# Kernel optimization log

Measured on AMD Instinct MI355X. Metric: run time of the kernel, lower is better.

The kernel has to match this reference:

```python
import jax, jax.numpy as jnp
import numpy as np

B, C, H, W = 64, 64, 128, 128
K = 7
PAD = 3


def setup_inputs() -> dict:
    key = jax.random.key(0)
    kx, kw, kb = jax.random.split(key, 3)
    scale = (C * K) ** (-0.5)
    x = jax.random.normal(kx, (B, C, H, W), dtype=jnp.float32)
    w = jax.random.normal(kw, (C, K, K), dtype=jnp.float32) * scale
    bias = jax.random.normal(kb, (1,), dtype=jnp.float32) * scale
    return {"x": x, "w": w, "bias": bias}


def reference(x, w, bias):
    # Single-output-channel 2D cross-correlation (sums over all input channels),
    # with zero padding PAD on both spatial dims, stride 1.
    # Matches the torch module's per-pixel loop: out[b, oh, ow] =
    #   sum_{c,dh,dw} x_pad[b, c, oh+dh, ow+dw] * w[c, dh, dw] + bias
    out = jax.lax.conv_general_dilated(
        x,                      # (B, C, H, W)
        w[None, :, :, :],       # (O=1, C, K, K)
        window_strides=(1, 1),
        padding=[(PAD, PAD), (PAD, PAD)],
        dimension_numbers=("NCHW", "OIHW", "NCHW"),
    )
    return out[:, 0] + bias  # (B, H_out, W_out)
```

## Files before the change

kernel.cpp:

```cpp
#include <hip/hip_runtime.h>
#include <stdint.h>


typedef short bf16x8 __attribute__((ext_vector_type(8)));
typedef float f32x4 __attribute__((ext_vector_type(4)));

#define HB    16
#define XS    20
#define XCOLS 134
#define XB1   (XCOLS * XS)
#define AROW  132
#define NSLOT 8

__device__ __forceinline__ uint32_t pk2bf(float a, float b) {
    uint32_t ua = __builtin_bit_cast(uint32_t, a);
    uint32_t ub = __builtin_bit_cast(uint32_t, b);
    ua += 0x7FFFu + ((ua >> 16) & 1u);
    ub += 0x7FFFu + ((ub >> 16) & 1u);
    return (ua >> 16) | (ub & 0xFFFF0000u);
}

__device__ __forceinline__ void lds_barrier() {
    asm volatile("s_waitcnt lgkmcnt(0)\n\ts_barrier" ::: "memory");
}

__global__ __launch_bounds__(256, 3)
void conv_v6(const float* __restrict__ x, const float* __restrict__ w,
             const float* __restrict__ bias, float* __restrict__ out) {
    __shared__ uint32_t xlds[2][2 * XB1];
    __shared__ float    acc[NSLOT * AROW];

    const int tid  = threadIdx.x;
    const int lane = tid & 63;
    const int wv   = tid >> 6;
    const int bx   = blockIdx.x;
    const int cs   = bx & 1;
    const int band = (bx >> 1) & 7;
    const int b    = bx >> 4;
    const int h0   = band * HB;
    const int r0   = h0 - 3;

    const int nl = lane & 15;
    const int q  = lane >> 4;

    for (int i = tid; i < NSLOT * AROW; i += 256) acc[i] = 0.f;
    for (int i = tid; i < 2 * 2 * 6 * XS; i += 256) {
        int bi   = i / (2 * 6 * XS);
        int rem  = i - bi * (2 * 6 * XS);
        int rs   = rem / (6 * XS);
        int rem2 = rem - rs * (6 * XS);
        int colh = rem2 / XS;
        int dwi  = rem2 - colh * XS;
        int col  = (colh < 3) ? colh : (128 + colh);
        xlds[bi][rs * XB1 + col * XS + dwi] = 0u;
    }

    bf16x8 Bf[7];
#pragma unroll
    for (int kk = 0; kk < 7; kk++) {
        bf16x8 f;
#pragma unroll
        for (int j = 0; j < 8; j++) {
            float v = (nl < 7) ? w[(32 * cs + 8 * q + j) * 49 + nl * 7 + kk] : 0.f;
            uint32_t u = __builtin_bit_cast(uint32_t, v);
            u += 0x7FFFu + ((u >> 16) & 1u);
            f[j] = (short)(u >> 16);
        }
        Bf[kk] = f;
    }

    const int cgrp = tid & 3;
    const int rsel = tid >> 7;
    const int colq = (tid >> 2) & 31;
    const float4* xp4 =
        (const float4*)x + ((size_t)b * 64 + 32 * cs + 8 * cgrp) * 4096;

    float4 pre[8];

    {
        const int r = r0 + rsel;
        const bool v = ((unsigned)r < 128u);
        const int base = r * 32 + colq;
#pragma unroll
        for (int i = 0; i < 8; i++) {
            float4 g = {0.f, 0.f, 0.f, 0.f};
            if (v) g = xp4[i * 4096 + base];
            pre[i] = g;
        }
#pragma unroll
        for (int j = 0; j < 4; j++) {
            float c0 = (&pre[0].x)[j], c1 = (&pre[1].x)[j], c2 = (&pre[2].x)[j],
                  c3 = (&pre[3].x)[j], c4 = (&pre[4].x)[j], c5 = (&pre[5].x)[j],
                  c6 = (&pre[6].x)[j], c7 = (&pre[7].x)[j];
            uint4 u;
            u.x = pk2bf(c0, c1); u.y = pk2bf(c2, c3);
            u.z = pk2bf(c4, c5); u.w = pk2bf(c6, c7);
            *(uint4*)&xlds[0][rsel * XB1 + (4 * colq + j + 3) * XS + 4 * cgrp] = u;
        }
        const int rn = r0 + 2 + rsel;
        const bool vn = ((unsigned)rn < 128u);
        const int basen = rn * 32 + colq;
#pragma unroll
        for (int i = 0; i < 8; i++) {
            float4 g = {0.f, 0.f, 0.f, 0.f};
            if (vn) g = xp4[i * 4096 + basen];
            pre[i] = g;
        }
    }
    lds_barrier();

    const float bv = (cs == 0) ? bias[0] : 0.f;

#pragma unroll 1
    for (int k = 0; k < 11; k++) {
        const uint32_t* buf = xlds[k & 1];

#pragma unroll
        for (int sub = 0; sub < 2; sub++) {
            const int r = r0 + 2 * k + sub;
            f32x4 a0 = {0.f, 0.f, 0.f, 0.f};
            f32x4 a1 = {0.f, 0.f, 0.f, 0.f};
            const uint32_t* rowbuf = buf + sub * XB1;
#pragma unroll
            for (int kk = 0; kk < 7; kk++) {
                const uint32_t* ap = &rowbuf[(32 * wv + nl + kk) * XS + 4 * q];
                uint4 A0 = *(const uint4*)ap;
                uint4 A1 = *(const uint4*)(ap + 16 * XS);
                a0 = __builtin_amdgcn_mfma_f32_16x16x32_bf16(
                         __builtin_bit_cast(bf16x8, A0), Bf[kk], a0, 0, 0, 0);
                a1 = __builtin_amdgcn_mfma_f32_16x16x32_bf16(
                         __builtin_bit_cast(bf16x8, A1), Bf[kk], a1, 0, 0, 0);
            }
            if (nl < 7) {
                const int oh = r + 3 - nl;
                if ((unsigned)(oh - h0) < (unsigned)HB) {
                    const int s = oh & 7;
                    float* p0 = &acc[s * AROW + 32 * wv + 4 * q];
                    f32x4 c0 = *(f32x4*)p0;
                    f32x4 c1 = *(f32x4*)(p0 + 16);
#pragma unroll
                    for (int j = 0; j < 4; j++) { c0[j] += a0[j]; c1[j] += a1[j]; }
                    *(f32x4*)p0 = c0;
                    *(f32x4*)(p0 + 16) = c1;
                }
            }
        }

        if (k >= 3) {
            const int oh  = r0 + 2 * k - 3 + (lane >> 5);
            const int col = 32 * wv + (lane & 31);
            float* ap = &acc[(oh & 7) * AROW + col];
            float v = *ap + bv;
            *ap = 0.f;
            atomicAdd(&out[(size_t)b * 16384 + oh * 128 + col], v);
        }

        if (k <= 9) {
            uint32_t* nbuf = xlds[(k + 1) & 1];
#pragma unroll
            for (int j = 0; j < 4; j++) {
                float c0 = (&pre[0].x)[j], c1 = (&pre[1].x)[j], c2 = (&pre[2].x)[j],
                      c3 = (&pre[3].x)[j], c4 = (&pre[4].x)[j], c5 = (&pre[5].x)[j],
                      c6 = (&pre[6].x)[j], c7 = (&pre[7].x)[j];
                uint4 u;
                u.x = pk2bf(c0, c1); u.y = pk2bf(c2, c3);
                u.z = pk2bf(c4, c5); u.w = pk2bf(c6, c7);
                *(uint4*)&nbuf[rsel * XB1 + (4 * colq + j + 3) * XS + 4 * cgrp] = u;
            }
            if (k <= 8) {
                const int rn = r0 + 2 * (k + 2) + rsel;
                const bool vn = ((unsigned)rn < 128u);
                const int basen = rn * 32 + colq;
#pragma unroll
                for (int i = 0; i < 8; i++) {
                    float4 g = {0.f, 0.f, 0.f, 0.f};
                    if (vn) g = xp4[i * 4096 + basen];
                    pre[i] = g;
                }
            }
        }

        lds_barrier();
    }
}

extern "C" void kernel_launch(void* const* d_in, const int* in_sizes, int n_in,
                              void* d_out, int out_size, void* d_ws, size_t ws_size,
                              hipStream_t stream) {
    const float* x    = (const float*)d_in[0];
    const float* w    = (const float*)d_in[1];
    const float* bias = (const float*)d_in[2];
    float* out        = (float*)d_out;

    hipMemsetAsync(d_out, 0, (size_t)out_size * sizeof(float), stream);
    hipLaunchKernelGGL(conv_v6, dim3(1024), dim3(256), 0, stream, x, w, bias, out);
}
```

Baseline: 373.3 us.

## Merge channel-split blocks so each block covers all 64 channels, dropping atomics and memset

Each block now processes both 32-channel halves, alternating between the two LDS buffers with separate weight fragment sets. The accumulated rows are written directly to the output, so the memset and the atomicAdd reduction are no longer needed. The grid halves to 512 blocks and the launch-bounds occupancy hint drops from 3 to 2 to make room for the second weight register set. In exchange there are fewer blocks, less parallelism, and an extra barrier per row pair.

```diff
diff --git a/kernel.cpp b/kernel.cpp
--- a/kernel.cpp
+++ b/kernel.cpp
@@ -24,8 +24,71 @@
     asm volatile("s_waitcnt lgkmcnt(0)\n\ts_barrier" ::: "memory");
 }
 
-__global__ __launch_bounds__(256, 3)
-void conv_v6(const float* __restrict__ x, const float* __restrict__ w,
+#define STAGE(DST)                                                            \
+    do {                                                                      \
+        _Pragma("unroll")                                                     \
+        for (int j = 0; j < 4; j++) {                                         \
+            float c0 = (&pre[0].x)[j], c1 = (&pre[1].x)[j],                   \
+                  c2 = (&pre[2].x)[j], c3 = (&pre[3].x)[j],                   \
+                  c4 = (&pre[4].x)[j], c5 = (&pre[5].x)[j],                   \
+                  c6 = (&pre[6].x)[j], c7 = (&pre[7].x)[j];                   \
+            uint4 u;                                                          \
+            u.x = pk2bf(c0, c1); u.y = pk2bf(c2, c3);                         \
+            u.z = pk2bf(c4, c5); u.w = pk2bf(c6, c7);                         \
+            *(uint4*)&(DST)[rsel * XB1 + (4 * colq + j + 3) * XS + 4 * cgrp] = u; \
+        }                                                                     \
+    } while (0)
+
+#define LOADPRE(XP, RK)                                                       \
+    do {                                                                      \
+        const int rn    = r0 + 2 * (RK) + rsel;                               \
+        const bool vn   = ((unsigned)rn < 128u);                              \
+        const int basen = rn * 32 + colq;                                     \
+        _Pragma("unroll")                                                     \
+        for (int i = 0; i < 8; i++) {                                         \
+            float4 g = {0.f, 0.f, 0.f, 0.f};                                  \
+            if (vn) g = (XP)[i * 4096 + basen];                               \
+            pre[i] = g;                                                       \
+        }                                                                     \
+    } while (0)
+
+#define MFMA_UNIT(BUF, BF)                                                    \
+    do {                                                                      \
+        _Pragma("unroll")                                                     \
+        for (int sub = 0; sub < 2; sub++) {                                   \
+            const int r = r0 + 2 * k2 + sub;                                  \
+            f32x4 a0 = {0.f, 0.f, 0.f, 0.f};                                  \
+            f32x4 a1 = {0.f, 0.f, 0.f, 0.f};                                  \
+            const uint32_t* rowbuf = (BUF) + sub * XB1;                       \
+            _Pragma("unroll")                                                 \
+            for (int kk = 0; kk < 7; kk++) {                                  \
+                const uint32_t* ap = &rowbuf[(32 * wv + nl + kk) * XS + 4 * q]; \
+                uint4 A0 = *(const uint4*)ap;                                 \
+                uint4 A1 = *(const uint4*)(ap + 16 * XS);                     \
+                a0 = __builtin_amdgcn_mfma_f32_16x16x32_bf16(                 \
+                         __builtin_bit_cast(bf16x8, A0), (BF)[kk], a0, 0, 0, 0); \
+                a1 = __builtin_amdgcn_mfma_f32_16x16x32_bf16(                 \
+                         __builtin_bit_cast(bf16x8, A1), (BF)[kk], a1, 0, 0, 0); \
+            }                                                                 \
+             \
+            if (nl < 7) {                                                     \
+                const int oh = r + 3 - nl;                                    \
+                if ((unsigned)(oh - h0) < (unsigned)HB) {                     \
+                    const int s = oh & 7;                                     \
+                    float* p0 = &acc[s * AROW + 32 * wv + 4 * q];             \
+                    f32x4 c0 = *(f32x4*)p0;                                   \
+                    f32x4 c1 = *(f32x4*)(p0 + 16);                            \
+                    _Pragma("unroll")                                         \
+                    for (int j = 0; j < 4; j++) { c0[j] += a0[j]; c1[j] += a1[j]; } \
+                    *(f32x4*)p0 = c0;                                         \
+                    *(f32x4*)(p0 + 16) = c1;                                  \
+                }                                                             \
+            }                                                                 \
+        }                                                                     \
+    } while (0)
+
+__global__ __launch_bounds__(256, 2)
+void conv_v7(const float* __restrict__ x, const float* __restrict__ w,
              const float* __restrict__ bias, float* __restrict__ out) {
     __shared__ uint32_t xlds[2][2 * XB1];
     __shared__ float    acc[NSLOT * AROW];
@@ -34,9 +97,8 @@
     const int lane = tid & 63;
     const int wv   = tid >> 6;
     const int bx   = blockIdx.x;
-    const int cs   = bx & 1;
-    const int band = (bx >> 1) & 7;
-    const int b    = bx >> 4;
+    const int band = bx & 7;
+    const int b    = bx >> 3;
     const int h0   = band * HB;
     const int r0   = h0 - 3;
 
@@ -55,131 +117,77 @@
         xlds[bi][rs * XB1 + col * XS + dwi] = 0u;
     }
 
-    bf16x8 Bf[7];
+    bf16x8 Bf0[7], Bf1[7];
 #pragma unroll
     for (int kk = 0; kk < 7; kk++) {
-        bf16x8 f;
+        bf16x8 f0, f1;
 #pragma unroll
         for (int j = 0; j < 8; j++) {
-            float v = (nl < 7) ? w[(32 * cs + 8 * q + j) * 49 + nl * 7 + kk] : 0.f;
-            uint32_t u = __builtin_bit_cast(uint32_t, v);
-            u += 0x7FFFu + ((u >> 16) & 1u);
-            f[j] = (short)(u >> 16);
-        }
-        Bf[kk] = f;
+            float v0 = (nl < 7) ? w[(8 * q + j) * 49 + nl * 7 + kk] : 0.f;
+            float v1 = (nl < 7) ? w[(32 + 8 * q + j) * 49 + nl * 7 + kk] : 0.f;
+            uint32_t u0 = __builtin_bit_cast(uint32_t, v0);
+            uint32_t u1 = __builtin_bit_cast(uint32_t, v1);
+            u0 += 0x7FFFu + ((u0 >> 16) & 1u);
+            u1 += 0x7FFFu + ((u1 >> 16) & 1u);
+            f0[j] = (short)(u0 >> 16);
+            f1[j] = (short)(u1 >> 16);
+        }
+        Bf0[kk] = f0;
+        Bf1[kk] = f1;
     }
 
     const int cgrp = tid & 3;
     const int rsel = tid >> 7;
     const int colq = (tid >> 2) & 31;
-    const float4* xp4 =
-        (const float4*)x + ((size_t)b * 64 + 32 * cs + 8 * cgrp) * 4096;
+    const float4* xp0 = (const float4*)x + ((size_t)b * 64 + 8 * cgrp) * 4096;
+    const float4* xp1 = xp0 + 32 * 4096;
 
     float4 pre[8];
 
     {
-        const int r = r0 + rsel;
-        const bool v = ((unsigned)r < 128u);
+        const int r    = r0 + rsel;
+        const bool v   = ((unsigned)r < 128u);
         const int base = r * 32 + colq;
 #pragma unroll
         for (int i = 0; i < 8; i++) {
             float4 g = {0.f, 0.f, 0.f, 0.f};
-            if (v) g = xp4[i * 4096 + base];
+            if (v) g = xp0[i * 4096 + base];
             pre[i] = g;
         }
-#pragma unroll
-        for (int j = 0; j < 4; j++) {
-            float c0 = (&pre[0].x)[j], c1 = (&pre[1].x)[j], c2 = (&pre[2].x)[j],
-                  c3 = (&pre[3].x)[j], c4 = (&pre[4].x)[j], c5 = (&pre[5].x)[j],
-                  c6 = (&pre[6].x)[j], c7 = (&pre[7].x)[j];
-            uint4 u;
-            u.x = pk2bf(c0, c1); u.y = pk2bf(c2, c3);
-            u.z = pk2bf(c4, c5); u.w = pk2bf(c6, c7);
-            *(uint4*)&xlds[0][rsel * XB1 + (4 * colq + j + 3) * XS + 4 * cgrp] = u;
-        }
-        const int rn = r0 + 2 + rsel;
-        const bool vn = ((unsigned)rn < 128u);
-        const int basen = rn * 32 + colq;
+        STAGE(xlds[0]);
 #pragma unroll
         for (int i = 0; i < 8; i++) {
             float4 g = {0.f, 0.f, 0.f, 0.f};
-            if (vn) g = xp4[i * 4096 + basen];
+            if (v) g = xp1[i * 4096 + base];
             pre[i] = g;
         }
     }
     lds_barrier();
 
-    const float bv = (cs == 0) ? bias[0] : 0.f;
+    const float bv = bias[0];
 
 #pragma unroll 1
-    for (int k = 0; k < 11; k++) {
-        const uint32_t* buf = xlds[k & 1];
-
-#pragma unroll
-        for (int sub = 0; sub < 2; sub++) {
-            const int r = r0 + 2 * k + sub;
-            f32x4 a0 = {0.f, 0.f, 0.f, 0.f};
-            f32x4 a1 = {0.f, 0.f, 0.f, 0.f};
-            const uint32_t* rowbuf = buf + sub * XB1;
-#pragma unroll
-            for (int kk = 0; kk < 7; kk++) {
-                const uint32_t* ap = &rowbuf[(32 * wv + nl + kk) * XS + 4 * q];
-                uint4 A0 = *(const uint4*)ap;
-                uint4 A1 = *(const uint4*)(ap + 16 * XS);
-                a0 = __builtin_amdgcn_mfma_f32_16x16x32_bf16(
-                         __builtin_bit_cast(bf16x8, A0), Bf[kk], a0, 0, 0, 0);
-                a1 = __builtin_amdgcn_mfma_f32_16x16x32_bf16(
-                         __builtin_bit_cast(bf16x8, A1), Bf[kk], a1, 0, 0, 0);
-            }
-            if (nl < 7) {
-                const int oh = r + 3 - nl;
-                if ((unsigned)(oh - h0) < (unsigned)HB) {
-                    const int s = oh & 7;
-                    float* p0 = &acc[s * AROW + 32 * wv + 4 * q];
-                    f32x4 c0 = *(f32x4*)p0;
-                    f32x4 c1 = *(f32x4*)(p0 + 16);
-#pragma unroll
-                    for (int j = 0; j < 4; j++) { c0[j] += a0[j]; c1[j] += a1[j]; }
-                    *(f32x4*)p0 = c0;
-                    *(f32x4*)(p0 + 16) = c1;
-                }
-            }
-        }
-
-        if (k >= 3) {
-            const int oh  = r0 + 2 * k - 3 + (lane >> 5);
+    for (int k2 = 0; k2 < 11; k2++) {
+        MFMA_UNIT(xlds[0], Bf0);
+        STAGE(xlds[1]);
+        if (k2 <= 9) LOADPRE(xp0, k2 + 1);
+        lds_barrier();
+
+        MFMA_UNIT(xlds[1], Bf1);
+
+        if (k2 >= 3) {
+            const int oh  = h0 + 2 * k2 - 6 + (lane >> 5);
             const int col = 32 * wv + (lane & 31);
             float* ap = &acc[(oh & 7) * AROW + col];
             float v = *ap + bv;
             *ap = 0.f;
-            atomicAdd(&out[(size_t)b * 16384 + oh * 128 + col], v);
-        }
-
-        if (k <= 9) {
-            uint32_t* nbuf = xlds[(k + 1) & 1];
-#pragma unroll
-            for (int j = 0; j < 4; j++) {
-                float c0 = (&pre[0].x)[j], c1 = (&pre[1].x)[j], c2 = (&pre[2].x)[j],
-                      c3 = (&pre[3].x)[j], c4 = (&pre[4].x)[j], c5 = (&pre[5].x)[j],
-                      c6 = (&pre[6].x)[j], c7 = (&pre[7].x)[j];
-                uint4 u;
-                u.x = pk2bf(c0, c1); u.y = pk2bf(c2, c3);
-                u.z = pk2bf(c4, c5); u.w = pk2bf(c6, c7);
-                *(uint4*)&nbuf[rsel * XB1 + (4 * colq + j + 3) * XS + 4 * cgrp] = u;
-            }
-            if (k <= 8) {
-                const int rn = r0 + 2 * (k + 2) + rsel;
-                const bool vn = ((unsigned)rn < 128u);
-                const int basen = rn * 32 + colq;
-#pragma unroll
-                for (int i = 0; i < 8; i++) {
-                    float4 g = {0.f, 0.f, 0.f, 0.f};
-                    if (vn) g = xp4[i * 4096 + basen];
-                    pre[i] = g;
-                }
-            }
-        }
-
+            out[(size_t)b * 16384 + (size_t)oh * 128 + col] = v;
+        }
+
+        if (k2 <= 9) {
+            STAGE(xlds[0]);
+            LOADPRE(xp1, k2 + 1);
+        }
         lds_barrier();
     }
 }
@@ -192,6 +200,5 @@
     const float* bias = (const float*)d_in[2];
     float* out        = (float*)d_out;
 
-    hipMemsetAsync(d_out, 0, (size_t)out_size * sizeof(float), stream);
-    hipLaunchKernelGGL(conv_v6, dim3(1024), dim3(256), 0, stream, x, w, bias, out);
-}
+    hipLaunchKernelGGL(conv_v7, dim3(512), dim3(256), 0, stream, x, w, bias, out);
+}
```

Result: no change. 379.5 us (+1.7%).

## Double row band height and use 512-thread blocks with one MFMA tile per wave

Applied to the files above, without the earlier changes.

Each block now covers 32 output rows instead of 16, and there are half as many blocks, so fewer input halo rows are reloaded per output row. Blocks grow to 512 threads (8 waves), each wave owning 16 columns with a single MFMA accumulator. Each thread stages 4 channels instead of 8, which cuts register pressure per thread. The trade-off is fewer blocks (512), a longer serial loop with more barriers, and half the MFMA work per wave between syncs.

```diff
diff --git a/kernel.cpp b/kernel.cpp
--- a/kernel.cpp
+++ b/kernel.cpp
@@ -5,7 +5,8 @@
 typedef short bf16x8 __attribute__((ext_vector_type(8)));
 typedef float f32x4 __attribute__((ext_vector_type(4)));
 
-#define HB    16
+#define HB    32
+#define NPAIR 19
 #define XS    20
 #define XCOLS 134
 #define XB1   (XCOLS * XS)
@@ -24,8 +25,34 @@
     asm volatile("s_waitcnt lgkmcnt(0)\n\ts_barrier" ::: "memory");
 }
 
-__global__ __launch_bounds__(256, 3)
-void conv_v6(const float* __restrict__ x, const float* __restrict__ w,
+#define STAGE(DST)                                                            \
+    do {                                                                      \
+        _Pragma("unroll")                                                     \
+        for (int j = 0; j < 4; j++) {                                         \
+            float c0 = (&pre[0].x)[j], c1 = (&pre[1].x)[j],                   \
+                  c2 = (&pre[2].x)[j], c3 = (&pre[3].x)[j];                   \
+            uint2 u;                                                          \
+            u.x = pk2bf(c0, c1);                                              \
+            u.y = pk2bf(c2, c3);                                              \
+            *(uint2*)&(DST)[rsel * XB1 + (4 * colq + j + 3) * XS + 2 * cgrp] = u; \
+        }                                                                     \
+    } while (0)
+
+#define LOADPRE(RK)                                                           \
+    do {                                                                      \
+        const int rn    = r0 + 2 * (RK) + rsel;                               \
+        const bool vn   = ((unsigned)rn < 128u);                              \
+        const int basen = rn * 32 + colq;                                     \
+        _Pragma("unroll")                                                     \
+        for (int i = 0; i < 4; i++) {                                         \
+            float4 g = {0.f, 0.f, 0.f, 0.f};                                  \
+            if (vn) g = xp4[i * 4096 + basen];                                \
+            pre[i] = g;                                                       \
+        }                                                                     \
+    } while (0)
+
+__global__ __launch_bounds__(512, 4)
+void conv_v8(const float* __restrict__ x, const float* __restrict__ w,
              const float* __restrict__ bias, float* __restrict__ out) {
     __shared__ uint32_t xlds[2][2 * XB1];
     __shared__ float    acc[NSLOT * AROW];
@@ -35,16 +62,16 @@
     const int wv   = tid >> 6;
     const int bx   = blockIdx.x;
     const int cs   = bx & 1;
-    const int band = (bx >> 1) & 7;
-    const int b    = bx >> 4;
+    const int band = (bx >> 1) & 3;
+    const int b    = bx >> 3;
     const int h0   = band * HB;
     const int r0   = h0 - 3;
 
     const int nl = lane & 15;
     const int q  = lane >> 4;
 
-    for (int i = tid; i < NSLOT * AROW; i += 256) acc[i] = 0.f;
-    for (int i = tid; i < 2 * 2 * 6 * XS; i += 256) {
+    for (int i = tid; i < NSLOT * AROW; i += 512) acc[i] = 0.f;
+    for (int i = tid; i < 2 * 2 * 6 * XS; i += 512) {
         int bi   = i / (2 * 6 * XS);
         int rem  = i - bi * (2 * 6 * XS);
         int rs   = rem / (6 * XS);
@@ -69,115 +96,62 @@
         Bf[kk] = f;
     }
 
-    const int cgrp = tid & 3;
-    const int rsel = tid >> 7;
-    const int colq = (tid >> 2) & 31;
+    const int cgrp = tid & 7;
+    const int colq = (tid >> 3) & 31;
+    const int rsel = tid >> 8;
     const float4* xp4 =
-        (const float4*)x + ((size_t)b * 64 + 32 * cs + 8 * cgrp) * 4096;
+        (const float4*)x + ((size_t)b * 64 + 32 * cs + 4 * cgrp) * 4096;
 
-    float4 pre[8];
+    float4 pre[4];
 
-    {
-        const int r = r0 + rsel;
-        const bool v = ((unsigned)r < 128u);
-        const int base = r * 32 + colq;
-#pragma unroll
-        for (int i = 0; i < 8; i++) {
-            float4 g = {0.f, 0.f, 0.f, 0.f};
-            if (v) g = xp4[i * 4096 + base];
-            pre[i] = g;
-        }
-#pragma unroll
-        for (int j = 0; j < 4; j++) {
-            float c0 = (&pre[0].x)[j], c1 = (&pre[1].x)[j], c2 = (&pre[2].x)[j],
-                  c3 = (&pre[3].x)[j], c4 = (&pre[4].x)[j], c5 = (&pre[5].x)[j],
-                  c6 = (&pre[6].x)[j], c7 = (&pre[7].x)[j];
-            uint4 u;
-            u.x = pk2bf(c0, c1); u.y = pk2bf(c2, c3);
-            u.z = pk2bf(c4, c5); u.w = pk2bf(c6, c7);
-            *(uint4*)&xlds[0][rsel * XB1 + (4 * colq + j + 3) * XS + 4 * cgrp] = u;
-        }
-        const int rn = r0 + 2 + rsel;
-        const bool vn = ((unsigned)rn < 128u);
-        const int basen = rn * 32 + colq;
-#pragma unroll
-        for (int i = 0; i < 8; i++) {
-            float4 g = {0.f, 0.f, 0.f, 0.f};
-            if (vn) g = xp4[i * 4096 + basen];
-            pre[i] = g;
-        }
-    }
+    LOADPRE(0);
+    STAGE(xlds[0]);
+    LOADPRE(1);
     lds_barrier();
 
     const float bv = (cs == 0) ? bias[0] : 0.f;
 
 #pragma unroll 1
-    for (int k = 0; k < 11; k++) {
+    for (int k = 0; k < NPAIR; k++) {
         const uint32_t* buf = xlds[k & 1];
 
 #pragma unroll
         for (int sub = 0; sub < 2; sub++) {
             const int r = r0 + 2 * k + sub;
             f32x4 a0 = {0.f, 0.f, 0.f, 0.f};
-            f32x4 a1 = {0.f, 0.f, 0.f, 0.f};
             const uint32_t* rowbuf = buf + sub * XB1;
 #pragma unroll
             for (int kk = 0; kk < 7; kk++) {
-                const uint32_t* ap = &rowbuf[(32 * wv + nl + kk) * XS + 4 * q];
+                const uint32_t* ap = &rowbuf[(16 * wv + nl + kk) * XS + 4 * q];
                 uint4 A0 = *(const uint4*)ap;
-                uint4 A1 = *(const uint4*)(ap + 16 * XS);
                 a0 = __builtin_amdgcn_mfma_f32_16x16x32_bf16(
                          __builtin_bit_cast(bf16x8, A0), Bf[kk], a0, 0, 0, 0);
-                a1 = __builtin_amdgcn_mfma_f32_16x16x32_bf16(
-                         __builtin_bit_cast(bf16x8, A1), Bf[kk], a1, 0, 0, 0);
             }
             if (nl < 7) {
                 const int oh = r + 3 - nl;
                 if ((unsigned)(oh - h0) < (unsigned)HB) {
                     const int s = oh & 7;
-                    float* p0 = &acc[s * AROW + 32 * wv + 4 * q];
+                    float* p0 = &acc[s * AROW + 16 * wv + 4 * q];
                     f32x4 c0 = *(f32x4*)p0;
-                    f32x4 c1 = *(f32x4*)(p0 + 16);
 #pragma unroll
-                    for (int j = 0; j < 4; j++) { c0[j] += a0[j]; c1[j] += a1[j]; }
+                    for (int j = 0; j < 4; j++) c0[j] += a0[j];
                     *(f32x4*)p0 = c0;
-                    *(f32x4*)(p0 + 16) = c1;
                 }
             }
         }
 
-        if (k >= 3) {
-            const int oh  = r0 + 2 * k - 3 + (lane >> 5);
-            const int col = 32 * wv + (lane & 31);
+        if (k >= 3 && lane < 32) {
+            const int oh  = h0 + 2 * k - 6 + (lane >> 4);
+            const int col = 16 * wv + (lane & 15);
             float* ap = &acc[(oh & 7) * AROW + col];
             float v = *ap + bv;
             *ap = 0.f;
-            atomicAdd(&out[(size_t)b * 16384 + oh * 128 + col], v);
+            atomicAdd(&out[(size_t)b * 16384 + (size_t)oh * 128 + col], v);
         }
 
-        if (k <= 9) {
-            uint32_t* nbuf = xlds[(k + 1) & 1];
-#pragma unroll
-            for (int j = 0; j < 4; j++) {
-                float c0 = (&pre[0].x)[j], c1 = (&pre[1].x)[j], c2 = (&pre[2].x)[j],
-                      c3 = (&pre[3].x)[j], c4 = (&pre[4].x)[j], c5 = (&pre[5].x)[j],
-                      c6 = (&pre[6].x)[j], c7 = (&pre[7].x)[j];
-                uint4 u;
-                u.x = pk2bf(c0, c1); u.y = pk2bf(c2, c3);
-                u.z = pk2bf(c4, c5); u.w = pk2bf(c6, c7);
-                *(uint4*)&nbuf[rsel * XB1 + (4 * colq + j + 3) * XS + 4 * cgrp] = u;
-            }
-            if (k <= 8) {
-                const int rn = r0 + 2 * (k + 2) + rsel;
-                const bool vn = ((unsigned)rn < 128u);
-                const int basen = rn * 32 + colq;
-#pragma unroll
-                for (int i = 0; i < 8; i++) {
-                    float4 g = {0.f, 0.f, 0.f, 0.f};
-                    if (vn) g = xp4[i * 4096 + basen];
-                    pre[i] = g;
-                }
-            }
+        if (k <= NPAIR - 2) {
+            STAGE(xlds[(k + 1) & 1]);
+            if (k <= NPAIR - 3) LOADPRE(k + 2);
         }
 
         lds_barrier();
@@ -193,5 +167,5 @@
     float* out        = (float*)d_out;
 
     hipMemsetAsync(d_out, 0, (size_t)out_size * sizeof(float), stream);
-    hipLaunchKernelGGL(conv_v6, dim3(1024), dim3(256), 0, stream, x, w, bias, out);
+    hipLaunchKernelGGL(conv_v8, dim3(512), dim3(512), 0, stream, x, w, bias, out);
 }
```

Result: no change. 376.9 us (+1.0%).
